# Performance work log

Hardware: AMD Instinct MI355X
Metric: run time of the kernel (lower is better)

## Reference

```python
import jax, jax.numpy as jnp
import numpy as np

B, C, H, W = 16, 256, 48, 48
QD, KD, VD = 64, 64, 256


def setup_inputs() -> dict:
    key = jax.random.key(0)
    ks = jax.random.split(key, 6)
    s = 0.02
    return {
        "x": jax.random.normal(ks[0], (B, C, H, W), dtype=jnp.float32),
        "Wq": jax.random.normal(ks[1], (QD, C), dtype=jnp.float32) * s,
        "bq": jnp.zeros((QD,), dtype=jnp.float32),
        "Wk": jax.random.normal(ks[2], (KD, C), dtype=jnp.float32) * s,
        "bk": jnp.zeros((KD,), dtype=jnp.float32),
        "Wv": jax.random.normal(ks[3], (VD, C), dtype=jnp.float32) * s,
        "bv": jnp.zeros((VD,), dtype=jnp.float32),
        "Wo": jax.random.normal(ks[4], (C, VD), dtype=jnp.float32) * s,
        "bo": jnp.zeros((C,), dtype=jnp.float32),
        # torch init is gamma=0 (identity residual); use 0.5 so output/grads are non-trivial
        "gamma": jnp.full((1,), 0.5, dtype=jnp.float32),
    }


def reference(x, Wq, bq, Wk, bk, Wv, bv, Wo, bo, gamma):
    b, c, h, w = x.shape
    n = h * w
    xf = x.reshape(b, c, n)  # [B,C,N]
    # 1x1 convs == per-pixel channel matmuls
    q = jnp.einsum('oc,bcn->bon', Wq, xf) + bq[None, :, None]  # [B,QD,N]
    k = jnp.einsum('oc,bcn->bon', Wk, xf) + bk[None, :, None]  # [B,KD,N]
    # energy[b,i,j] = <q[:,i], k[:,j]>  (no scaling in original)
    energy = jnp.einsum('bqi,bqj->bij', q, k)  # [B,N,N]
    attention = jax.nn.softmax(energy, axis=-1)
    v = jnp.einsum('oc,bcn->bon', Wv, xf) + bv[None, :, None]  # [B,VD,N]
    # out = bmm(value, attention^T): out[:, :, i] = sum_j v[:, :, j] * attn[i, j]
    o = jnp.einsum('bvj,bij->bvi', v, attention)  # [B,VD,N]
    o = jnp.einsum('oc,bcn->bon', Wo, o) + bo[None, :, None]  # [B,C,N]
    out = gamma[0] * o.reshape(b, c, h, w) + x
    return out, attention
```

## Files before the change

kernel.cpp:

```cpp
#include <hip/hip_runtime.h>

#define B_ 16
#define C_ 256
#define N_ 2304
#define QD_ 64
#define VD_ 256

typedef unsigned short u16;
typedef __attribute__((ext_vector_type(8))) short bf16x8;
typedef __attribute__((ext_vector_type(4))) float f32x4;
typedef __attribute__((ext_vector_type(4))) u16 u16x4;

__device__ inline u16 f2b(float f){
  unsigned u = __builtin_bit_cast(unsigned, f);
  return (u16)((u + 0x7FFFu + ((u >> 16) & 1u)) >> 16);
}

__global__ void prep_weights(const float* __restrict__ Wq, const float* __restrict__ Wk,
                             const float* __restrict__ Wv, const float* __restrict__ Wo,
                             u16* __restrict__ W_all, u16* __restrict__ Wo_bf){
  int i = blockIdx.x * 256 + threadIdx.x;
  int row = i >> 8;
  float val;
  if (row < 64) val = Wq[i];
  else if (row < 128) val = Wk[i - 64*C_];
  else val = Wv[i - 128*C_];
  W_all[i] = f2b(val);
  if (i < C_*VD_) Wo_bf[i] = f2b(Wo[i]);
}

__global__ void transpose_x(const float* __restrict__ x, u16* __restrict__ x_t){
  __shared__ float tile[64][65];
  int b = blockIdx.z;
  int c0 = blockIdx.y * 64, n0 = blockIdx.x * 64;
  int tx = threadIdx.x & 63, ty = threadIdx.x >> 6;
  const float* xb = x + (size_t)b * C_ * N_;
  #pragma unroll
  for (int rr = 0; rr < 16; ++rr){
    int c = ty*16 + rr;
    tile[c][tx] = xb[(size_t)(c0 + c) * N_ + n0 + tx];
  }
  __syncthreads();
  u16* xtb = x_t + (size_t)b * N_ * C_;
  #pragma unroll
  for (int rr = 0; rr < 16; ++rr){
    int n = ty*16 + rr;
    xtb[(size_t)(n0 + n) * C_ + c0 + tx] = f2b(tile[tx][n]);
  }
}

template<int KD>
__device__ inline void mfma_tile64(const u16* __restrict__ A, const u16* __restrict__ Bt,
                                   f32x4 acc[4][4], int lane){
  int cl = lane & 15, q = lane >> 4;
  const u16* ab = A + cl*KD + q*8;
  const u16* bb = Bt + cl*KD + q*8;
  for (int kk = 0; kk < KD/32; ++kk){
    bf16x8 a[4], bfr[4];
    #pragma unroll
    for (int t = 0; t < 4; ++t) a[t] = *(const bf16x8*)(ab + t*16*KD + kk*32);
    #pragma unroll
    for (int t = 0; t < 4; ++t) bfr[t] = *(const bf16x8*)(bb + t*16*KD + kk*32);
    #pragma unroll
    for (int tm = 0; tm < 4; ++tm)
      #pragma unroll
      for (int tn = 0; tn < 4; ++tn)
        acc[tm][tn] = __builtin_amdgcn_mfma_f32_16x16x32_bf16(a[tm], bfr[tn], acc[tm][tn], 0, 0, 0);
  }
}

__global__ __launch_bounds__(512) void qkv_gemm(const u16* __restrict__ W_all, const u16* __restrict__ x_t,
    const float* __restrict__ bq, const float* __restrict__ bk, const float* __restrict__ bv,
    u16* __restrict__ q_t, u16* __restrict__ k_t, u16* __restrict__ v){
  int b = blockIdx.z;
  int lane = threadIdx.x & 63, wid = threadIdx.x >> 6;
  int m0 = blockIdx.x*128 + (wid >> 2)*64;
  int n0 = blockIdx.y*256 + (wid & 3)*64;
  const u16* xtb = x_t + (size_t)b*N_*C_;
  f32x4 acc[4][4] = {};
  mfma_tile64<C_>(W_all + (size_t)m0*C_, xtb + (size_t)n0*C_, acc, lane);
  int cl = lane & 15, q = lane >> 4;
  size_t qb = (size_t)b*N_*QD_;
  u16* vb = v + (size_t)b*VD_*N_;
  #pragma unroll
  for (int tm = 0; tm < 4; ++tm){
    int m = m0 + tm*16 + q*4;
    #pragma unroll
    for (int tn = 0; tn < 4; ++tn){
      int n = n0 + tn*16 + cl;
      f32x4 d = acc[tm][tn];
      if (m0 < 64){
        u16x4 pk;
        #pragma unroll
        for (int r = 0; r < 4; ++r) pk[r] = f2b(d[r] + bq[m + r]);
        *(u16x4*)(q_t + qb + (size_t)n*QD_ + m) = pk;
      } else if (m0 < 128){
        u16x4 pk;
        #pragma unroll
        for (int r = 0; r < 4; ++r) pk[r] = f2b(d[r] + bk[m - 64 + r]);
        *(u16x4*)(k_t + qb + (size_t)n*QD_ + (m - 64)) = pk;
      } else {
        #pragma unroll
        for (int r = 0; r < 4; ++r) vb[(size_t)(m - 128 + r)*N_ + n] = f2b(d[r] + bv[m - 128 + r]);
      }
    }
  }
}

__global__ __launch_bounds__(512) void energy_gemm(const u16* __restrict__ q_t, const u16* __restrict__ k_t,
                                                   float* __restrict__ attn){
  int b = blockIdx.z;
  int lane = threadIdx.x & 63, wid = threadIdx.x >> 6;
  int i0 = blockIdx.x*128 + (wid >> 2)*64;
  int j0 = blockIdx.y*256 + (wid & 3)*64;
  size_t qb = (size_t)b*N_*QD_;
  f32x4 acc[4][4] = {};
  mfma_tile64<QD_>(q_t + qb + (size_t)i0*QD_, k_t + qb + (size_t)j0*QD_, acc, lane);
  float* ab = attn + (size_t)b*N_*N_;
  int cl = lane & 15, q = lane >> 4;
  #pragma unroll
  for (int tm = 0; tm < 4; ++tm){
    int i = i0 + tm*16 + q*4;
    #pragma unroll
    for (int tn = 0; tn < 4; ++tn){
      int j = j0 + tn*16 + cl;
      #pragma unroll
      for (int r = 0; r < 4; ++r) ab[(size_t)(i + r)*N_ + j] = acc[tm][tn][r];
    }
  }
}

__global__ __launch_bounds__(256) void softmax_rows(float* __restrict__ attn){
  int i = blockIdx.x, b = blockIdx.y;
  float* row = attn + ((size_t)b*N_ + i)*N_;
  int t = threadIdx.x;
  int lane = t & 63, wid = t >> 6;
  float v[9];
  float mx = -3.0e38f;
  #pragma unroll
  for (int k = 0; k < 9; ++k){ v[k] = row[t + k*256]; mx = fmaxf(mx, v[k]); }
  #pragma unroll
  for (int off = 1; off < 64; off <<= 1) mx = fmaxf(mx, __shfl_xor(mx, off));
  __shared__ float redm[4], reds[4];
  if (lane == 0) redm[wid] = mx;
  __syncthreads();
  mx = fmaxf(fmaxf(redm[0], redm[1]), fmaxf(redm[2], redm[3]));
  float s = 0.f;
  #pragma unroll
  for (int k = 0; k < 9; ++k){ v[k] = __expf(v[k] - mx); s += v[k]; }
  #pragma unroll
  for (int off = 1; off < 64; off <<= 1) s += __shfl_xor(s, off);
  if (lane == 0) reds[wid] = s;
  __syncthreads();
  s = reds[0] + reds[1] + reds[2] + reds[3];
  float inv = 1.0f / s;
  #pragma unroll
  for (int k = 0; k < 9; ++k) row[t + k*256] = v[k] * inv;
}

__device__ inline bf16x8 pack8(f32x4 lo, f32x4 hi){
  bf16x8 r;
  #pragma unroll
  for (int i = 0; i < 4; ++i){ r[i] = (short)f2b(lo[i]); r[i+4] = (short)f2b(hi[i]); }
  return r;
}

__global__ __launch_bounds__(512) void pv_gemm(const float* __restrict__ attn, const u16* __restrict__ v,
                                               u16* __restrict__ o_t){
  int b = blockIdx.z;
  int lane = threadIdx.x & 63, wid = threadIdx.x >> 6;
  int i0 = blockIdx.x*128 + (wid >> 2)*64;
  int vd0 = (wid & 3)*64;
  const float* ab = attn + (size_t)b*N_*N_;
  const u16* vb = v + (size_t)b*VD_*N_;
  int cl = lane & 15, q = lane >> 4;
  const float* arow = ab + (size_t)(i0 + cl)*N_ + q*8;
  const u16* bb = vb + (size_t)(vd0 + cl)*N_ + q*8;
  f32x4 acc[4][4] = {};
  for (int kk = 0; kk < N_/32; ++kk){
    bf16x8 a[4], bfr[4];
    #pragma unroll
    for (int t = 0; t < 4; ++t){
      const float* p = arow + (size_t)t*16*N_ + kk*32;
      a[t] = pack8(*(const f32x4*)p, *(const f32x4*)(p + 4));
    }
    #pragma unroll
    for (int t = 0; t < 4; ++t) bfr[t] = *(const bf16x8*)(bb + (size_t)t*16*N_ + kk*32);
    #pragma unroll
    for (int tm = 0; tm < 4; ++tm)
      #pragma unroll
      for (int tn = 0; tn < 4; ++tn)
        acc[tm][tn] = __builtin_amdgcn_mfma_f32_16x16x32_bf16(a[tm], bfr[tn], acc[tm][tn], 0, 0, 0);
  }
  u16* ob = o_t + (size_t)b*N_*VD_;
  #pragma unroll
  for (int tm = 0; tm < 4; ++tm){
    int i = i0 + tm*16 + q*4;
    #pragma unroll
    for (int tn = 0; tn < 4; ++tn){
      int vd = vd0 + tn*16 + cl;
      #pragma unroll
      for (int r = 0; r < 4; ++r) ob[(size_t)(i + r)*VD_ + vd] = f2b(acc[tm][tn][r]);
    }
  }
}

__global__ __launch_bounds__(512) void out_gemm(const u16* __restrict__ Wo_bf, const u16* __restrict__ o_t,
    const float* __restrict__ bo, const float* __restrict__ gamma,
    const float* __restrict__ x, float* __restrict__ out){
  int b = blockIdx.z;
  int lane = threadIdx.x & 63, wid = threadIdx.x >> 6;
  int c0 = blockIdx.x*128 + (wid >> 2)*64;
  int n0 = blockIdx.y*256 + (wid & 3)*64;
  f32x4 acc[4][4] = {};
  mfma_tile64<VD_>(Wo_bf + (size_t)c0*VD_, o_t + (size_t)b*N_*VD_ + (size_t)n0*VD_, acc, lane);
  float g = gamma[0];
  const float* xb = x + (size_t)b*C_*N_;
  float* ob = out + (size_t)b*C_*N_;
  int cl = lane & 15, q = lane >> 4;
  #pragma unroll
  for (int tm = 0; tm < 4; ++tm){
    int c = c0 + tm*16 + q*4;
    #pragma unroll
    for (int tn = 0; tn < 4; ++tn){
      int n = n0 + tn*16 + cl;
      #pragma unroll
      for (int r = 0; r < 4; ++r){
        size_t idx = (size_t)(c + r)*N_ + n;
        ob[idx] = g*(acc[tm][tn][r] + bo[c + r]) + xb[idx];
      }
    }
  }
}

extern "C" void kernel_launch(void* const* d_in, const int* in_sizes, int n_in,
                              void* d_out, int out_size, void* d_ws, size_t ws_size,
                              hipStream_t stream){
  const float* x     = (const float*)d_in[0];
  const float* Wq    = (const float*)d_in[1];
  const float* bq    = (const float*)d_in[2];
  const float* Wk    = (const float*)d_in[3];
  const float* bk    = (const float*)d_in[4];
  const float* Wv    = (const float*)d_in[5];
  const float* bv    = (const float*)d_in[6];
  const float* Wo    = (const float*)d_in[7];
  const float* bo    = (const float*)d_in[8];
  const float* gamma = (const float*)d_in[9];

  float* out  = (float*)d_out;
  float* attn = out + (size_t)B_*C_*N_;

  char* ws = (char*)d_ws;
  u16* W_all = (u16*)(ws + 0);
  u16* Wo_bf = (u16*)(ws + 196608);
  u16* x_t   = (u16*)(ws + 327680);
  u16* q_t   = (u16*)(ws + 19202048);
  u16* k_t   = (u16*)(ws + 23920640);
  u16* v     = (u16*)(ws + 28639232);
  u16* o_t   = (u16*)(ws + 47513600);

  prep_weights<<<dim3(384), 256, 0, stream>>>(Wq, Wk, Wv, Wo, W_all, Wo_bf);
  transpose_x<<<dim3(36, 4, 16), 256, 0, stream>>>(x, x_t);
  qkv_gemm<<<dim3(3, 9, 16), 512, 0, stream>>>(W_all, x_t, bq, bk, bv, q_t, k_t, v);
  energy_gemm<<<dim3(18, 9, 16), 512, 0, stream>>>(q_t, k_t, attn);
  softmax_rows<<<dim3(2304, 16), 256, 0, stream>>>(attn);
  pv_gemm<<<dim3(18, 1, 16), 512, 0, stream>>>(attn, v, o_t);
  out_gemm<<<dim3(2, 9, 16), 512, 0, stream>>>(Wo_bf, o_t, bo, gamma, x, out);
}
```

Before: 1.068 ms.

## Emit bf16 attention copy from softmax and feed PV GEMM from it

The softmax kernel now uses 576 threads with one float4 per thread, and writes both the fp32 attention (a required output) and a bf16 copy into workspace. The PV GEMM reads this bf16 copy through the shared mfma_tile64 helper rather than reloading fp32 and converting inline. Its grid is split over two VD halves with 256-thread blocks. This halves the bytes PV reads from the large attention matrix, at the cost of an extra bf16 write in softmax.

```diff
diff --git a/kernel.cpp b/kernel.cpp
--- a/kernel.cpp
+++ b/kernel.cpp
@@ -130,69 +130,53 @@
   }
 }
 
-__global__ __launch_bounds__(256) void softmax_rows(float* __restrict__ attn){
+__global__ __launch_bounds__(576) void softmax_rows(float* __restrict__ attn, u16* __restrict__ attn_bf){
   int i = blockIdx.x, b = blockIdx.y;
-  float* row = attn + ((size_t)b*N_ + i)*N_;
+  size_t base = ((size_t)b*N_ + i)*N_;
+  float* row = attn + base;
+  u16* brow = attn_bf + base;
   int t = threadIdx.x;
   int lane = t & 63, wid = t >> 6;
-  float v[9];
-  float mx = -3.0e38f;
-  #pragma unroll
-  for (int k = 0; k < 9; ++k){ v[k] = row[t + k*256]; mx = fmaxf(mx, v[k]); }
+  f32x4 v = *(const f32x4*)(row + t*4);
+  float mx = fmaxf(fmaxf(v[0], v[1]), fmaxf(v[2], v[3]));
   #pragma unroll
   for (int off = 1; off < 64; off <<= 1) mx = fmaxf(mx, __shfl_xor(mx, off));
-  __shared__ float redm[4], reds[4];
+  __shared__ float redm[9], reds[9];
   if (lane == 0) redm[wid] = mx;
   __syncthreads();
-  mx = fmaxf(fmaxf(redm[0], redm[1]), fmaxf(redm[2], redm[3]));
+  mx = redm[0];
+  #pragma unroll
+  for (int k = 1; k < 9; ++k) mx = fmaxf(mx, redm[k]);
   float s = 0.f;
   #pragma unroll
-  for (int k = 0; k < 9; ++k){ v[k] = __expf(v[k] - mx); s += v[k]; }
+  for (int k = 0; k < 4; ++k){ v[k] = __expf(v[k] - mx); s += v[k]; }
   #pragma unroll
   for (int off = 1; off < 64; off <<= 1) s += __shfl_xor(s, off);
   if (lane == 0) reds[wid] = s;
   __syncthreads();
-  s = reds[0] + reds[1] + reds[2] + reds[3];
+  s = reds[0];
+  #pragma unroll
+  for (int k = 1; k < 9; ++k) s += reds[k];
   float inv = 1.0f / s;
-  #pragma unroll
-  for (int k = 0; k < 9; ++k) row[t + k*256] = v[k] * inv;
-}
-
-__device__ inline bf16x8 pack8(f32x4 lo, f32x4 hi){
-  bf16x8 r;
-  #pragma unroll
-  for (int i = 0; i < 4; ++i){ r[i] = (short)f2b(lo[i]); r[i+4] = (short)f2b(hi[i]); }
-  return r;
-}
-
-__global__ __launch_bounds__(512) void pv_gemm(const float* __restrict__ attn, const u16* __restrict__ v,
+  u16x4 pk;
+  #pragma unroll
+  for (int k = 0; k < 4; ++k){ v[k] *= inv; pk[k] = f2b(v[k]); }
+  *(f32x4*)(row + t*4) = v;
+  *(u16x4*)(brow + t*4) = pk;
+}
+
+__global__ __launch_bounds__(256) void pv_gemm(const u16* __restrict__ attn_bf, const u16* __restrict__ v,
                                                u16* __restrict__ o_t){
   int b = blockIdx.z;
   int lane = threadIdx.x & 63, wid = threadIdx.x >> 6;
-  int i0 = blockIdx.x*128 + (wid >> 2)*64;
-  int vd0 = (wid & 3)*64;
-  const float* ab = attn + (size_t)b*N_*N_;
+  int i0 = blockIdx.x*128 + (wid >> 1)*64;
+  int vd0 = blockIdx.y*128 + (wid & 1)*64;
+  const u16* ab = attn_bf + (size_t)b*N_*N_;
   const u16* vb = v + (size_t)b*VD_*N_;
-  int cl = lane & 15, q = lane >> 4;
-  const float* arow = ab + (size_t)(i0 + cl)*N_ + q*8;
-  const u16* bb = vb + (size_t)(vd0 + cl)*N_ + q*8;
-  f32x4 acc[4][4] = {};
-  for (int kk = 0; kk < N_/32; ++kk){
-    bf16x8 a[4], bfr[4];
-    #pragma unroll
-    for (int t = 0; t < 4; ++t){
-      const float* p = arow + (size_t)t*16*N_ + kk*32;
-      a[t] = pack8(*(const f32x4*)p, *(const f32x4*)(p + 4));
-    }
-    #pragma unroll
-    for (int t = 0; t < 4; ++t) bfr[t] = *(const bf16x8*)(bb + (size_t)t*16*N_ + kk*32);
-    #pragma unroll
-    for (int tm = 0; tm < 4; ++tm)
-      #pragma unroll
-      for (int tn = 0; tn < 4; ++tn)
-        acc[tm][tn] = __builtin_amdgcn_mfma_f32_16x16x32_bf16(a[tm], bfr[tn], acc[tm][tn], 0, 0, 0);
-  }
+  f32x4 acc[4][4] = {};
+  mfma_tile64<N_>(ab + (size_t)i0*N_, vb + (size_t)vd0*N_, acc, lane);
   u16* ob = o_t + (size_t)b*N_*VD_;
+  int cl = lane & 15, q = lane >> 4;
   #pragma unroll
   for (int tm = 0; tm < 4; ++tm){
     int i = i0 + tm*16 + q*4;
@@ -251,19 +235,20 @@
   float* attn = out + (size_t)B_*C_*N_;
 
   char* ws = (char*)d_ws;
-  u16* W_all = (u16*)(ws + 0);
-  u16* Wo_bf = (u16*)(ws + 196608);
-  u16* x_t   = (u16*)(ws + 327680);
-  u16* q_t   = (u16*)(ws + 19202048);
-  u16* k_t   = (u16*)(ws + 23920640);
-  u16* v     = (u16*)(ws + 28639232);
-  u16* o_t   = (u16*)(ws + 47513600);
+  u16* W_all   = (u16*)(ws + 0);
+  u16* Wo_bf   = (u16*)(ws + 196608);
+  u16* x_t     = (u16*)(ws + 327680);
+  u16* q_t     = (u16*)(ws + 19202048);
+  u16* k_t     = (u16*)(ws + 23920640);
+  u16* v       = (u16*)(ws + 28639232);
+  u16* o_t     = (u16*)(ws + 47513600);
+  u16* attn_bf = (u16*)(ws + 66387968);
 
   prep_weights<<<dim3(384), 256, 0, stream>>>(Wq, Wk, Wv, Wo, W_all, Wo_bf);
   transpose_x<<<dim3(36, 4, 16), 256, 0, stream>>>(x, x_t);
   qkv_gemm<<<dim3(3, 9, 16), 512, 0, stream>>>(W_all, x_t, bq, bk, bv, q_t, k_t, v);
   energy_gemm<<<dim3(18, 9, 16), 512, 0, stream>>>(q_t, k_t, attn);
-  softmax_rows<<<dim3(2304, 16), 256, 0, stream>>>(attn);
-  pv_gemm<<<dim3(18, 1, 16), 512, 0, stream>>>(attn, v, o_t);
+  softmax_rows<<<dim3(2304, 16), 576, 0, stream>>>(attn, attn_bf);
+  pv_gemm<<<dim3(18, 2, 16), 256, 0, stream>>>(attn_bf, v, o_t);
   out_gemm<<<dim3(2, 9, 16), 512, 0, stream>>>(Wo_bf, o_t, bo, gamma, x, out);
 }
```

Result: faster. 878.2 us (-17.7%).
